# Kernel tuning notes

Measured on AMD Instinct MI355X. Metric: run time of the kernel, lower is better.

## Reference

```python
import jax, jax.numpy as jnp
import numpy as np

# ---- constants derived from init_kwargs (grid_size, pc_range, d_bound) ----
_PC_MIN = np.array([-48.0, -48.0, -4.0])
_PC_MAX = np.array([48.0, 48.0, 4.0])
_VOX = np.array([0.75, 0.75, 2.0])
_D0, _DMAX, _DSTEP = 2.0, 50.0, 1.0
_NPTS = ((_PC_MAX - _PC_MIN) // _VOX).astype(np.int64)  # [128, 128, 4]
_axes = [np.linspace(mn, mx - s, n) + s / 2 for mn, mx, n, s in zip(_PC_MIN, _PC_MAX, _NPTS, _VOX)]
_g = np.stack(np.meshgrid(*_axes, indexing="ij"), axis=-1)  # [X,Y,Z,3]
GRID = jnp.asarray(np.concatenate([_g, np.ones((*_g.shape[:3], 1))], axis=-1), dtype=jnp.float32)  # [X,Y,Z,4] homogeneous


def _grid_sample_3d(inp, grid):
    # Trilinear grid_sample, align_corners=True, zero padding.
    # inp: [N,C,D,H,W]; grid: [N,X,Y,Z,3], last dim = (x->W, y->H, z->D).
    N, C, D, H, W = inp.shape
    ix = (grid[..., 0] + 1.0) * 0.5 * (W - 1)
    iy = (grid[..., 1] + 1.0) * 0.5 * (H - 1)
    iz = (grid[..., 2] + 1.0) * 0.5 * (D - 1)
    x0, y0, z0 = jnp.floor(ix), jnp.floor(iy), jnp.floor(iz)
    gather = jax.vmap(lambda f, zi, yi, xi: f[:, zi, yi, xi])  # per-sample fancy gather -> [C,X,Y,Z]
    out = jnp.zeros((N, C) + grid.shape[1:4], inp.dtype)
    for dz in (0, 1):
        for dy in (0, 1):
            for dx in (0, 1):
                xc, yc, zc = x0 + dx, y0 + dy, z0 + dz
                w = (1.0 - jnp.abs(ix - xc)) * (1.0 - jnp.abs(iy - yc)) * (1.0 - jnp.abs(iz - zc))
                valid = (xc >= 0) & (xc <= W - 1) & (yc >= 0) & (yc <= H - 1) & (zc >= 0) & (zc <= D - 1)
                xi = jnp.clip(xc, 0, W - 1).astype(jnp.int32)
                yi = jnp.clip(yc, 0, H - 1).astype(jnp.int32)
                zi = jnp.clip(zc, 0, D - 1).astype(jnp.int32)
                v = gather(inp, zi, yi, xi)  # [N,C,X,Y,Z]
                out = out + v * (w * valid)[:, None]
    return out


def _forward(frustum, intrinsics, lidar_to_sensor):
    B, Nc = intrinsics.shape[:2]
    # [B,N,D,H,W,C] -> [B*N, C, D, H, W]
    f = frustum.reshape((B * Nc,) + frustum.shape[2:]).transpose(0, 4, 1, 2, 3)
    D, H, W = f.shape[2], f.shape[3], f.shape[4]
    # grid points in sensor coords: solve(lidar_to_sensor, grid) == inv(lidar_to_sensor) @ grid
    inv = jnp.linalg.inv(lidar_to_sensor)  # [B,N,4,4]
    pts = jnp.einsum("bnij,xyzj->bnxyzi", inv, GRID)[..., :3]  # [B,N,X,Y,Z,3]
    uvd = jnp.einsum("bnij,bnxyzj->bnxyzi", intrinsics, pts)
    uv = uvd[..., :2] / uvd[..., 2:3]
    dbin = (uvd[..., 2:3] - _D0) / _DSTEP
    g = jnp.concatenate([uv, dbin], axis=-1).reshape((B * Nc,) + GRID.shape[:3] + (3,))
    g = 2.0 * g / jnp.asarray([W, H, D], g.dtype) - 1.0
    vox = _grid_sample_3d(f, g)  # [B*N, C, X, Y, Z]
    vox = vox.reshape((B, Nc, f.shape[1]) + GRID.shape[:3])
    # sum over cameras and Z, then [B,C,X,Y] -> [B,C,Y,X]
    return vox.sum(axis=(1, 5)).transpose(0, 1, 3, 2)


def setup_inputs() -> dict:
    key = jax.random.key(0)
    k1, k2, k3 = jax.random.split(key, 3)
    B, Nc, D, H, W, C = 2, 6, 48, 28, 60, 64
    frustum = jax.random.normal(k1, (B, Nc, D, H, W, C), jnp.float32)
    fl = 25.0 + 10.0 * jax.random.uniform(k2, (B, Nc), jnp.float32)  # feature-scale focal length
    intrinsics = jnp.zeros((B, Nc, 3, 3), jnp.float32)
    intrinsics = intrinsics.at[..., 0, 0].set(fl).at[..., 1, 1].set(fl)
    intrinsics = intrinsics.at[..., 0, 2].set(W / 2.0).at[..., 1, 2].set(H / 2.0).at[..., 2, 2].set(1.0)
    lidar_to_sensor = jnp.eye(4, dtype=jnp.float32) + 0.05 * jax.random.normal(k3, (B, Nc, 4, 4), jnp.float32)
    return {"frustum": frustum, "intrinsics": intrinsics, "lidar_to_sensor": lidar_to_sensor}


def reference(frustum, intrinsics, lidar_to_sensor):
    return _forward(frustum, intrinsics, lidar_to_sensor)
```

## Files before the change

kernel.cpp:

```cpp
#include <hip/hip_runtime.h>
#include <math.h>

#define B_DIM  2
#define NCAM   6
#define D_DIM  48
#define H_DIM  28
#define W_DIM  60
#define C_DIM  64
#define X_DIM  128
#define Y_DIM  128
#define Z_DIM  4
#define NCELL  (B_DIM * X_DIM * Y_DIM)
#define FR_CAM ((size_t)D_DIM * H_DIM * W_DIM * C_DIM)

__global__ __launch_bounds__(256) void frustum_to_bev_fused(
        const float* __restrict__ frustum,
        const float* __restrict__ intr,
        const float* __restrict__ l2s,
        float* __restrict__ out) {
    __shared__ float Ms[B_DIM * NCAM * 12];

    int t = threadIdx.x;
    if (t < B_DIM * NCAM) {
        float A[4][8];
        const float* L = l2s + t * 16;
        for (int i = 0; i < 4; i++) {
            for (int jj = 0; jj < 4; jj++) A[i][jj] = L[i * 4 + jj];
            for (int jj = 0; jj < 4; jj++) A[i][4 + jj] = (i == jj) ? 1.0f : 0.0f;
        }
        for (int col = 0; col < 4; col++) {
            int p = col;
            float mx = fabsf(A[col][col]);
            for (int r = col + 1; r < 4; r++) {
                float v = fabsf(A[r][col]);
                if (v > mx) { mx = v; p = r; }
            }
            if (p != col) {
                for (int jj = 0; jj < 8; jj++) {
                    float tmp = A[col][jj]; A[col][jj] = A[p][jj]; A[p][jj] = tmp;
                }
            }
            float inv = 1.0f / A[col][col];
            for (int jj = 0; jj < 8; jj++) A[col][jj] *= inv;
            for (int r = 0; r < 4; r++) {
                if (r == col) continue;
                float f = A[r][col];
                for (int jj = 0; jj < 8; jj++) A[r][jj] -= f * A[col][jj];
            }
        }
        const float* K = intr + t * 9;
        for (int r = 0; r < 3; r++) {
            for (int c = 0; c < 4; c++) {
                float s = 0.0f;
                for (int k = 0; k < 3; k++) s += K[r * 3 + k] * A[k][4 + c];
                Ms[t * 12 + r * 4 + c] = s;
            }
        }
    }
    __syncthreads();

    int wave = (blockIdx.x << 2) | (t >> 6);
    int lane = t & 63;
    int b = wave >> 14;
    int y = (wave >> 7) & 127;
    int x = wave & 127;

    float px = 0.75f * (float)x - 47.625f;
    float py = 0.75f * (float)y - 47.625f;

    int j  = (lane < NCAM * Z_DIM) ? lane : 0;
    int n  = j >> 2;
    int z  = j & 3;
    const float* m = &Ms[(b * NCAM + n) * 12];
    float pz = 2.0f * (float)z - 3.0f;
    float uu = m[0] * px + m[1] * py + m[2]  * pz + m[3];
    float vv = m[4] * px + m[5] * py + m[6]  * pz + m[7];
    float dd = m[8] * px + m[9] * py + m[10] * pz + m[11];

    float ix = (uu / dd) * (59.0f / 60.0f);
    float iy = (vv / dd) * (27.0f / 28.0f);
    float iz = (dd - 2.0f) * (47.0f / 48.0f);

    bool valid = (lane < NCAM * Z_DIM) &&
                 (ix > -1.0f) && (ix < 60.0f) &&
                 (iy > -1.0f) && (iy < 28.0f) &&
                 (iz > -1.0f) && (iz < 48.0f);

    float xf = floorf(ix), yf = floorf(iy), zf = floorf(iz);
    float fx = ix - xf, fy = iy - yf, fz = iz - zf;
    int packed = (n << 24) | ((((int)zf + 1) & 0xff) << 16)
               | ((((int)yf + 1) & 0xff) << 8) | (((int)xf + 1) & 0xff);

    unsigned long long mask = __ballot(valid);

    float acc = 0.0f;
    const float* fbase = frustum + (size_t)b * NCAM * FR_CAM + lane;

    while (mask) {
        int k = __ffsll(mask) - 1;
        mask &= mask - 1;
        int   pk  = __shfl(packed, k);
        float kfx = __shfl(fx, k);
        float kfy = __shfl(fy, k);
        float kfz = __shfl(fz, k);
        int kn = (pk >> 24) & 0xff;
        int zi = ((pk >> 16) & 0xff) - 1;
        int yi = ((pk >> 8)  & 0xff) - 1;
        int xi = (pk & 0xff) - 1;
        float wx[2] = {1.0f - kfx, kfx};
        float wy[2] = {1.0f - kfy, kfy};
        float wz[2] = {1.0f - kfz, kfz};

        const float* fb = fbase + (size_t)kn * FR_CAM;

#pragma unroll
        for (int dz = 0; dz < 2; dz++) {
            int zz = zi + dz;
            if (zz < 0 || zz > D_DIM - 1) continue;
#pragma unroll
            for (int dy = 0; dy < 2; dy++) {
                int yy = yi + dy;
                if (yy < 0 || yy > H_DIM - 1) continue;
                float wzy = wz[dz] * wy[dy];
#pragma unroll
                for (int dx = 0; dx < 2; dx++) {
                    int xx = xi + dx;
                    if (xx < 0 || xx > W_DIM - 1) continue;
                    float w = wzy * wx[dx];
                    acc += w * fb[(((size_t)zz * H_DIM + yy) * W_DIM + xx) * C_DIM];
                }
            }
        }
    }

    out[(((size_t)b * C_DIM + lane) * Y_DIM + y) * X_DIM + x] = acc;
}

extern "C" void kernel_launch(void* const* d_in, const int* in_sizes, int n_in,
                              void* d_out, int out_size, void* d_ws, size_t ws_size,
                              hipStream_t stream) {
    const float* frustum = (const float*)d_in[0];
    const float* intr    = (const float*)d_in[1];
    const float* l2s     = (const float*)d_in[2];
    float* out = (float*)d_out;

    frustum_to_bev_fused<<<NCELL / 4, 256, 0, stream>>>(frustum, intr, l2s, out);
}
```

Measured before the change: 314.7 us.

## Process four BEV cells per wave with interleaved gather streams and float4 store

Each wave now handles four adjacent x cells instead of one. Two lane halves compute projections for a pair of cells, and two ballots build four 24-bit masks. The gather loop round-robins across the four cells' sample lists, which exposes more independent loads per iteration and gives four accumulators. The result is written as a float4, and the grid shrinks by four. The matrix-inversion setup is also fully unrolled with branchless pivot swaps. The cost is higher register pressure and load imbalance when the four cells have different numbers of valid samples.

```diff
diff --git a/kernel.cpp b/kernel.cpp
--- a/kernel.cpp
+++ b/kernel.cpp
@@ -13,6 +13,37 @@
 #define NCELL  (B_DIM * X_DIM * Y_DIM)
 #define FR_CAM ((size_t)D_DIM * H_DIM * W_DIM * C_DIM)
 
+
+__device__ __forceinline__ void gather_one(float& acc, int pk, float kfx, float kfy, float kfz,
+                                           const float* __restrict__ fbase) {
+    int kn = (pk >> 24) & 0xff;
+    int zi = ((pk >> 16) & 0xff) - 1;
+    int yi = ((pk >> 8)  & 0xff) - 1;
+    int xi = (pk & 0xff) - 1;
+    float wx[2] = {1.0f - kfx, kfx};
+    float wy[2] = {1.0f - kfy, kfy};
+    float wz[2] = {1.0f - kfz, kfz};
+    const float* fb = fbase + (size_t)kn * FR_CAM;
+#pragma unroll
+    for (int dz = 0; dz < 2; dz++) {
+        int zz = zi + dz;
+        if (zz < 0 || zz > D_DIM - 1) continue;
+#pragma unroll
+        for (int dy = 0; dy < 2; dy++) {
+            int yy = yi + dy;
+            if (yy < 0 || yy > H_DIM - 1) continue;
+            float wzy = wz[dz] * wy[dy];
+#pragma unroll
+            for (int dx = 0; dx < 2; dx++) {
+                int xx = xi + dx;
+                if (xx < 0 || xx > W_DIM - 1) continue;
+                float w = wzy * wx[dx];
+                acc += w * fb[(((size_t)zz * H_DIM + yy) * W_DIM + xx) * C_DIM];
+            }
+        }
+    }
+}
+
 __global__ __launch_bounds__(256) void frustum_to_bev_fused(
         const float* __restrict__ frustum,
         const float* __restrict__ intr,
@@ -24,34 +55,50 @@
     if (t < B_DIM * NCAM) {
         float A[4][8];
         const float* L = l2s + t * 16;
+#pragma unroll
         for (int i = 0; i < 4; i++) {
+#pragma unroll
             for (int jj = 0; jj < 4; jj++) A[i][jj] = L[i * 4 + jj];
+#pragma unroll
             for (int jj = 0; jj < 4; jj++) A[i][4 + jj] = (i == jj) ? 1.0f : 0.0f;
         }
+#pragma unroll
         for (int col = 0; col < 4; col++) {
             int p = col;
             float mx = fabsf(A[col][col]);
+#pragma unroll
             for (int r = col + 1; r < 4; r++) {
                 float v = fabsf(A[r][col]);
                 if (v > mx) { mx = v; p = r; }
             }
-            if (p != col) {
+#pragma unroll
+            for (int r = col + 1; r < 4; r++) {
+                bool sw = (p == r);
+#pragma unroll
                 for (int jj = 0; jj < 8; jj++) {
-                    float tmp = A[col][jj]; A[col][jj] = A[p][jj]; A[p][jj] = tmp;
+                    float a = A[col][jj], bsw = A[r][jj];
+                    A[col][jj] = sw ? bsw : a;
+                    A[r][jj]   = sw ? a : bsw;
                 }
             }
             float inv = 1.0f / A[col][col];
+#pragma unroll
             for (int jj = 0; jj < 8; jj++) A[col][jj] *= inv;
+#pragma unroll
             for (int r = 0; r < 4; r++) {
                 if (r == col) continue;
                 float f = A[r][col];
+#pragma unroll
                 for (int jj = 0; jj < 8; jj++) A[r][jj] -= f * A[col][jj];
             }
         }
         const float* K = intr + t * 9;
+#pragma unroll
         for (int r = 0; r < 3; r++) {
+#pragma unroll
             for (int c = 0; c < 4; c++) {
                 float s = 0.0f;
+#pragma unroll
                 for (int k = 0; k < 3; k++) s += K[r * 3 + k] * A[k][4 + c];
                 Ms[t * 12 + r * 4 + c] = s;
             }
@@ -59,81 +106,106 @@
     }
     __syncthreads();
 
-    int wave = (blockIdx.x << 2) | (t >> 6);
+    int wg   = (blockIdx.x << 2) | (t >> 6);
     int lane = t & 63;
-    int b = wave >> 14;
-    int y = (wave >> 7) & 127;
-    int x = wave & 127;
-
-    float px = 0.75f * (float)x - 47.625f;
+    int cellbase = wg << 2;
+    int b  = cellbase >> 14;
+    int y  = (cellbase >> 7) & 127;
+    int x0 = cellbase & 127;
+
     float py = 0.75f * (float)y - 47.625f;
 
-    int j  = (lane < NCAM * Z_DIM) ? lane : 0;
-    int n  = j >> 2;
-    int z  = j & 3;
-    const float* m = &Ms[(b * NCAM + n) * 12];
+    int j = (lane < 48) ? lane : 0;
+    int q = (j >= 24) ? 1 : 0;
+    int s = j - 24 * q;
+    int n = s >> 2;
+    int z = s & 3;
     float pz = 2.0f * (float)z - 3.0f;
-    float uu = m[0] * px + m[1] * py + m[2]  * pz + m[3];
-    float vv = m[4] * px + m[5] * py + m[6]  * pz + m[7];
-    float dd = m[8] * px + m[9] * py + m[10] * pz + m[11];
-
-    float ix = (uu / dd) * (59.0f / 60.0f);
-    float iy = (vv / dd) * (27.0f / 28.0f);
-    float iz = (dd - 2.0f) * (47.0f / 48.0f);
-
-    bool valid = (lane < NCAM * Z_DIM) &&
-                 (ix > -1.0f) && (ix < 60.0f) &&
-                 (iy > -1.0f) && (iy < 28.0f) &&
-                 (iz > -1.0f) && (iz < 48.0f);
-
-    float xf = floorf(ix), yf = floorf(iy), zf = floorf(iz);
-    float fx = ix - xf, fy = iy - yf, fz = iz - zf;
-    int packed = (n << 24) | ((((int)zf + 1) & 0xff) << 16)
-               | ((((int)yf + 1) & 0xff) << 8) | (((int)xf + 1) & 0xff);
-
-    unsigned long long mask = __ballot(valid);
-
-    float acc = 0.0f;
+
+    const float* mm = &Ms[(b * NCAM + n) * 12];
+    float M0 = mm[0], M1 = mm[1], M2 = mm[2],  M3  = mm[3];
+    float M4 = mm[4], M5 = mm[5], M6 = mm[6],  M7  = mm[7];
+    float M8 = mm[8], M9 = mm[9], M10 = mm[10], M11 = mm[11];
+
+    int pA, pB;
+    float fxA, fyA, fzA, fxB, fyB, fzB;
+    unsigned mk0, mk1, mk2, mk3;
+
+    {
+        int xc = x0 + q;
+        float px = 0.75f * (float)xc - 47.625f;
+        float uu = M0 * px + M1 * py + M2  * pz + M3;
+        float vv = M4 * px + M5 * py + M6  * pz + M7;
+        float dd = M8 * px + M9 * py + M10 * pz + M11;
+        float ix = (uu / dd) * (59.0f / 60.0f);
+        float iy = (vv / dd) * (27.0f / 28.0f);
+        float iz = (dd - 2.0f) * (47.0f / 48.0f);
+        bool valid = (lane < 48) &&
+                     (ix > -1.0f) && (ix < 60.0f) &&
+                     (iy > -1.0f) && (iy < 28.0f) &&
+                     (iz > -1.0f) && (iz < 48.0f);
+        float xf = floorf(ix), yf = floorf(iy), zf = floorf(iz);
+        fxA = ix - xf; fyA = iy - yf; fzA = iz - zf;
+        pA = (n << 24) | ((((int)zf + 1) & 0xff) << 16)
+           | ((((int)yf + 1) & 0xff) << 8) | (((int)xf + 1) & 0xff);
+        unsigned long long bl = __ballot(valid);
+        mk0 = (unsigned)(bl & 0xffffffULL);
+        mk1 = (unsigned)((bl >> 24) & 0xffffffULL);
+    }
+    {
+        int xc = x0 + 2 + q;
+        float px = 0.75f * (float)xc - 47.625f;
+        float uu = M0 * px + M1 * py + M2  * pz + M3;
+        float vv = M4 * px + M5 * py + M6  * pz + M7;
+        float dd = M8 * px + M9 * py + M10 * pz + M11;
+        float ix = (uu / dd) * (59.0f / 60.0f);
+        float iy = (vv / dd) * (27.0f / 28.0f);
+        float iz = (dd - 2.0f) * (47.0f / 48.0f);
+        bool valid = (lane < 48) &&
+                     (ix > -1.0f) && (ix < 60.0f) &&
+                     (iy > -1.0f) && (iy < 28.0f) &&
+                     (iz > -1.0f) && (iz < 48.0f);
+        float xf = floorf(ix), yf = floorf(iy), zf = floorf(iz);
+        fxB = ix - xf; fyB = iy - yf; fzB = iz - zf;
+        pB = (n << 24) | ((((int)zf + 1) & 0xff) << 16)
+           | ((((int)yf + 1) & 0xff) << 8) | (((int)xf + 1) & 0xff);
+        unsigned long long bl = __ballot(valid);
+        mk2 = (unsigned)(bl & 0xffffffULL);
+        mk3 = (unsigned)((bl >> 24) & 0xffffffULL);
+    }
+
+    float acc0 = 0.0f, acc1 = 0.0f, acc2 = 0.0f, acc3 = 0.0f;
     const float* fbase = frustum + (size_t)b * NCAM * FR_CAM + lane;
 
-    while (mask) {
-        int k = __ffsll(mask) - 1;
-        mask &= mask - 1;
-        int   pk  = __shfl(packed, k);
-        float kfx = __shfl(fx, k);
-        float kfy = __shfl(fy, k);
-        float kfz = __shfl(fz, k);
-        int kn = (pk >> 24) & 0xff;
-        int zi = ((pk >> 16) & 0xff) - 1;
-        int yi = ((pk >> 8)  & 0xff) - 1;
-        int xi = (pk & 0xff) - 1;
-        float wx[2] = {1.0f - kfx, kfx};
-        float wy[2] = {1.0f - kfy, kfy};
-        float wz[2] = {1.0f - kfz, kfz};
-
-        const float* fb = fbase + (size_t)kn * FR_CAM;
-
-#pragma unroll
-        for (int dz = 0; dz < 2; dz++) {
-            int zz = zi + dz;
-            if (zz < 0 || zz > D_DIM - 1) continue;
-#pragma unroll
-            for (int dy = 0; dy < 2; dy++) {
-                int yy = yi + dy;
-                if (yy < 0 || yy > H_DIM - 1) continue;
-                float wzy = wz[dz] * wy[dy];
-#pragma unroll
-                for (int dx = 0; dx < 2; dx++) {
-                    int xx = xi + dx;
-                    if (xx < 0 || xx > W_DIM - 1) continue;
-                    float w = wzy * wx[dx];
-                    acc += w * fb[(((size_t)zz * H_DIM + yy) * W_DIM + xx) * C_DIM];
-                }
-            }
-        }
-    }
-
-    out[(((size_t)b * C_DIM + lane) * Y_DIM + y) * X_DIM + x] = acc;
+    while (mk0 | mk1 | mk2 | mk3) {
+        if (mk0) {
+            int k = __ffs(mk0) - 1; mk0 &= mk0 - 1;
+            int   pk  = __shfl(pA, k);
+            float a = __shfl(fxA, k), bb = __shfl(fyA, k), cc = __shfl(fzA, k);
+            gather_one(acc0, pk, a, bb, cc, fbase);
+        }
+        if (mk1) {
+            int k = __ffs(mk1) + 23; mk1 &= mk1 - 1;
+            int   pk  = __shfl(pA, k);
+            float a = __shfl(fxA, k), bb = __shfl(fyA, k), cc = __shfl(fzA, k);
+            gather_one(acc1, pk, a, bb, cc, fbase);
+        }
+        if (mk2) {
+            int k = __ffs(mk2) - 1; mk2 &= mk2 - 1;
+            int   pk  = __shfl(pB, k);
+            float a = __shfl(fxB, k), bb = __shfl(fyB, k), cc = __shfl(fzB, k);
+            gather_one(acc2, pk, a, bb, cc, fbase);
+        }
+        if (mk3) {
+            int k = __ffs(mk3) + 23; mk3 &= mk3 - 1;
+            int   pk  = __shfl(pB, k);
+            float a = __shfl(fxB, k), bb = __shfl(fyB, k), cc = __shfl(fzB, k);
+            gather_one(acc3, pk, a, bb, cc, fbase);
+        }
+    }
+
+    float4 v4 = make_float4(acc0, acc1, acc2, acc3);
+    *reinterpret_cast<float4*>(out + ((((size_t)b * C_DIM + lane) * Y_DIM + y) * X_DIM + x0)) = v4;
 }
 
 extern "C" void kernel_launch(void* const* d_in, const int* in_sizes, int n_in,
@@ -144,5 +216,5 @@
     const float* l2s     = (const float*)d_in[2];
     float* out = (float*)d_out;
 
-    frustum_to_bev_fused<<<NCELL / 4, 256, 0, stream>>>(frustum, intr, l2s, out);
+    frustum_to_bev_fused<<<NCELL / 16, 256, 0, stream>>>(frustum, intr, l2s, out);
 }
```

Measured after the change: 368.0 us. 1.17x slower.

## Software-pipeline trilinear gathers and coalesce output stores through shared memory

Applied to the files above, without the earlier changes.

The gather loop now issues all eight corner loads for the next valid sample (with clamped indices and masked weights instead of branches) before consuming the previous sample's loads, so memory latency overlaps with accumulation. Output writes are staged through a shared buffer so each block writes four consecutive x positions per channel instead of stride-X scattered stores. The matrix inverse is fully unrolled with branchless pivot swaps. This costs more registers and always loads eight corners even when some fall out of bounds.

```diff
diff --git a/kernel.cpp b/kernel.cpp
--- a/kernel.cpp
+++ b/kernel.cpp
@@ -13,45 +13,114 @@
 #define NCELL  (B_DIM * X_DIM * Y_DIM)
 #define FR_CAM ((size_t)D_DIM * H_DIM * W_DIM * C_DIM)
 
+
+__device__ __forceinline__ void gather_issue(float* v, int pk,
+                                             const float* __restrict__ fbase) {
+    int kn = (pk >> 24) & 0xff;
+    int zi = ((pk >> 16) & 0xff) - 1;
+    int yi = ((pk >> 8)  & 0xff) - 1;
+    int xi = (pk & 0xff) - 1;
+    const float* fb = fbase + (size_t)kn * FR_CAM;
+#pragma unroll
+    for (int dz = 0; dz < 2; dz++) {
+        int zc = min(max(zi + dz, 0), D_DIM - 1);
+#pragma unroll
+        for (int dy = 0; dy < 2; dy++) {
+            int yc = min(max(yi + dy, 0), H_DIM - 1);
+#pragma unroll
+            for (int dx = 0; dx < 2; dx++) {
+                int xc = min(max(xi + dx, 0), W_DIM - 1);
+                v[dz * 4 + dy * 2 + dx] =
+                    fb[(((size_t)zc * H_DIM + yc) * W_DIM + xc) * C_DIM];
+            }
+        }
+    }
+}
+
+__device__ __forceinline__ void gather_consume(float& acc, const float* v, int pk,
+                                               float kfx, float kfy, float kfz) {
+    int zi = ((pk >> 16) & 0xff) - 1;
+    int yi = ((pk >> 8)  & 0xff) - 1;
+    int xi = (pk & 0xff) - 1;
+    float wx[2] = {1.0f - kfx, kfx};
+    float wy[2] = {1.0f - kfy, kfy};
+    float wz[2] = {1.0f - kfz, kfz};
+#pragma unroll
+    for (int dz = 0; dz < 2; dz++) {
+        int zz = zi + dz;
+        bool bz = (zz >= 0) && (zz <= D_DIM - 1);
+#pragma unroll
+        for (int dy = 0; dy < 2; dy++) {
+            int yy = yi + dy;
+            bool by = (yy >= 0) && (yy <= H_DIM - 1);
+            float wzy = wz[dz] * wy[dy];
+#pragma unroll
+            for (int dx = 0; dx < 2; dx++) {
+                int xx = xi + dx;
+                bool bx = (xx >= 0) && (xx <= W_DIM - 1);
+                float w = (bz && by && bx) ? (wzy * wx[dx]) : 0.0f;
+                acc += w * v[dz * 4 + dy * 2 + dx];
+            }
+        }
+    }
+}
+
 __global__ __launch_bounds__(256) void frustum_to_bev_fused(
         const float* __restrict__ frustum,
         const float* __restrict__ intr,
         const float* __restrict__ l2s,
         float* __restrict__ out) {
     __shared__ float Ms[B_DIM * NCAM * 12];
+    __shared__ float accs[4][65];
 
     int t = threadIdx.x;
     if (t < B_DIM * NCAM) {
         float A[4][8];
         const float* L = l2s + t * 16;
+#pragma unroll
         for (int i = 0; i < 4; i++) {
+#pragma unroll
             for (int jj = 0; jj < 4; jj++) A[i][jj] = L[i * 4 + jj];
+#pragma unroll
             for (int jj = 0; jj < 4; jj++) A[i][4 + jj] = (i == jj) ? 1.0f : 0.0f;
         }
+#pragma unroll
         for (int col = 0; col < 4; col++) {
             int p = col;
             float mx = fabsf(A[col][col]);
+#pragma unroll
             for (int r = col + 1; r < 4; r++) {
                 float v = fabsf(A[r][col]);
                 if (v > mx) { mx = v; p = r; }
             }
-            if (p != col) {
+#pragma unroll
+            for (int r = col + 1; r < 4; r++) {
+                bool sw = (p == r);
+#pragma unroll
                 for (int jj = 0; jj < 8; jj++) {
-                    float tmp = A[col][jj]; A[col][jj] = A[p][jj]; A[p][jj] = tmp;
+                    float a = A[col][jj], bsw = A[r][jj];
+                    A[col][jj] = sw ? bsw : a;
+                    A[r][jj]   = sw ? a : bsw;
                 }
             }
             float inv = 1.0f / A[col][col];
+#pragma unroll
             for (int jj = 0; jj < 8; jj++) A[col][jj] *= inv;
+#pragma unroll
             for (int r = 0; r < 4; r++) {
                 if (r == col) continue;
                 float f = A[r][col];
+#pragma unroll
                 for (int jj = 0; jj < 8; jj++) A[r][jj] -= f * A[col][jj];
             }
         }
         const float* K = intr + t * 9;
+#pragma unroll
         for (int r = 0; r < 3; r++) {
+#pragma unroll
             for (int c = 0; c < 4; c++) {
                 float s = 0.0f;
+#pragma unroll
                 for (int k = 0; k < 3; k++) s += K[r * 3 + k] * A[k][4 + c];
                 Ms[t * 12 + r * 4 + c] = s;
             }
@@ -96,44 +165,36 @@
     float acc = 0.0f;
     const float* fbase = frustum + (size_t)b * NCAM * FR_CAM + lane;
 
-    while (mask) {
-        int k = __ffsll(mask) - 1;
-        mask &= mask - 1;
-        int   pk  = __shfl(packed, k);
-        float kfx = __shfl(fx, k);
-        float kfy = __shfl(fy, k);
-        float kfz = __shfl(fz, k);
-        int kn = (pk >> 24) & 0xff;
-        int zi = ((pk >> 16) & 0xff) - 1;
-        int yi = ((pk >> 8)  & 0xff) - 1;
-        int xi = (pk & 0xff) - 1;
-        float wx[2] = {1.0f - kfx, kfx};
-        float wy[2] = {1.0f - kfy, kfy};
-        float wz[2] = {1.0f - kfz, kfz};
-
-        const float* fb = fbase + (size_t)kn * FR_CAM;
-
-#pragma unroll
-        for (int dz = 0; dz < 2; dz++) {
-            int zz = zi + dz;
-            if (zz < 0 || zz > D_DIM - 1) continue;
-#pragma unroll
-            for (int dy = 0; dy < 2; dy++) {
-                int yy = yi + dy;
-                if (yy < 0 || yy > H_DIM - 1) continue;
-                float wzy = wz[dz] * wy[dy];
-#pragma unroll
-                for (int dx = 0; dx < 2; dx++) {
-                    int xx = xi + dx;
-                    if (xx < 0 || xx > W_DIM - 1) continue;
-                    float w = wzy * wx[dx];
-                    acc += w * fb[(((size_t)zz * H_DIM + yy) * W_DIM + xx) * C_DIM];
-                }
-            }
-        }
-    }
-
-    out[(((size_t)b * C_DIM + lane) * Y_DIM + y) * X_DIM + x] = acc;
+    if (mask) {
+        int k = __ffsll(mask) - 1; mask &= mask - 1;
+        int   cpk = __shfl(packed, k);
+        float cfx = __shfl(fx, k), cfy = __shfl(fy, k), cfz = __shfl(fz, k);
+        float cv[8];
+        gather_issue(cv, cpk, fbase);
+        while (mask) {
+            int k2 = __ffsll(mask) - 1; mask &= mask - 1;
+            int   npk = __shfl(packed, k2);
+            float nfx = __shfl(fx, k2), nfy = __shfl(fy, k2), nfz = __shfl(fz, k2);
+            float nv[8];
+            gather_issue(nv, npk, fbase);
+            gather_consume(acc, cv, cpk, cfx, cfy, cfz);
+            cpk = npk; cfx = nfx; cfy = nfy; cfz = nfz;
+#pragma unroll
+            for (int i = 0; i < 8; i++) cv[i] = nv[i];
+        }
+        gather_consume(acc, cv, cpk, cfx, cfy, cfz);
+    }
+
+    accs[t >> 6][lane] = acc;
+    __syncthreads();
+
+    int cellbase = blockIdx.x << 2;
+    int bb = cellbase >> 14;
+    int yy = (cellbase >> 7) & 127;
+    int x0 = cellbase & 127;
+    int c  = t >> 2;
+    int xi = t & 3;
+    out[(((size_t)bb * C_DIM + c) * Y_DIM + yy) * X_DIM + x0 + xi] = accs[xi][c];
 }
 
 extern "C" void kernel_launch(void* const* d_in, const int* in_sizes, int n_in,
```

Result: faster. 288.6 us (-8.3%).
